# Performance work log

Hardware: AMD Instinct MI355X
Metric: run time of the kernel (lower is better)

Reference implementation:

```python
import jax, jax.numpy as jnp
import numpy as np

L, D, DH, NH, P = 12, 768, 64, 12, 16
B, H_IMG, W_IMG = 16, 384, 384
MAX_GRID = 64


def setup_inputs() -> dict:
    key = jax.random.key(0)
    ks = jax.random.split(key, 10)
    r = lambda k, shp: (0.02 * jax.random.normal(k, shp, dtype=jnp.float32))
    return {
        "x": jax.random.normal(ks[0], (B, 3, H_IMG, W_IMG), dtype=jnp.float32),
        "conv_w": r(ks[1], (D, 3, P, P)),
        "conv_b": jnp.zeros((D,), jnp.float32),
        "ln_w": jnp.ones((D,), jnp.float32),
        "ln_b": jnp.zeros((D,), jnp.float32),
        "pos_y_emb": r(ks[2], (MAX_GRID, D)),
        "pos_x_emb": r(ks[3], (MAX_GRID, D)),
        "mha_ln_w": jnp.ones((L, D), jnp.float32),
        "mha_ln_b": jnp.zeros((L, D), jnp.float32),
        "qw": r(ks[4], (L, D, D)),
        "kw": r(ks[5], (L, D, D)),
        "vw": r(ks[6], (L, D, D)),
        "ffn_ln_w": jnp.ones((L, D), jnp.float32),
        "ffn_ln_b": jnp.zeros((L, D), jnp.float32),
        "w1": r(ks[7], (L, D, 4 * D)),
        "b1": jnp.zeros((L, 4 * D), jnp.float32),
        "w2": r(ks[8], (L, 4 * D, D)),
        "b2": jnp.zeros((L, D), jnp.float32),
        "x_shift": 0,
        "y_shift": 0,
    }


def _ln(x, w, b):
    m = jnp.mean(x, axis=-1, keepdims=True)
    v = jnp.var(x, axis=-1, keepdims=True)
    return (x - m) * jax.lax.rsqrt(v + 1e-5) * w + b


def reference(x, conv_w, conv_b, ln_w, ln_b, pos_y_emb, pos_x_emb,
              mha_ln_w, mha_ln_b, qw, kw, vw,
              ffn_ln_w, ffn_ln_b, w1, b1, w2, b2, x_shift, y_shift):
    # patch embed: conv + relu, to NHWC, layernorm
    h = jax.lax.conv_general_dilated(x, conv_w, (P, P), 'VALID',
                                     dimension_numbers=('NCHW', 'OIHW', 'NCHW'))
    h = jax.nn.relu(h + conv_b[None, :, None, None])
    h = jnp.transpose(h, (0, 2, 3, 1))  # [B, GH, GW, D]
    h = _ln(h, ln_w, ln_b)
    b, gh, gw, d = h.shape
    n = gh * gw
    # 2D factorized positional embedding, shared layernorm
    pos = (pos_y_emb[jnp.arange(gh) + y_shift][:, None, :]
           + pos_x_emb[jnp.arange(gw) + x_shift][None, :, :])  # [GH, GW, D]
    pos = _ln(pos, ln_w, ln_b).reshape(1, n, d)
    pos_emb = jnp.broadcast_to(pos, (b, n, d))
    t = h.reshape(b, n, d) + pos_emb
    scale = 1.0 / jnp.sqrt(jnp.float32(DH))
    for i in range(L):
        # pre-LN MHA (no output projection, mask=None / pretrain=False)
        tl = _ln(t, mha_ln_w[i], mha_ln_b[i])
        q = (tl @ qw[i]).reshape(b, n, NH, DH).transpose(0, 2, 1, 3)
        k = (tl @ kw[i]).reshape(b, n, NH, DH).transpose(0, 2, 1, 3)
        v = (tl @ vw[i]).reshape(b, n, NH, DH).transpose(0, 2, 1, 3)
        attn = jax.nn.softmax(jnp.einsum('bhqd,bhkd->bhqk', q, k) * scale, axis=-1)
        o = jnp.einsum('bhqk,bhkd->bhqd', attn, v).transpose(0, 2, 1, 3).reshape(b, n, d)
        t = t + o
        fl = _ln(t, ffn_ln_w[i], ffn_ln_b[i])
        t = t + (jax.nn.relu(fl @ w1[i] + b1[i]) @ w2[i] + b2[i])
    return t, pos_emb
```

## Files before the change

kernel.cpp:

```cpp
#include <hip/hip_runtime.h>

typedef unsigned short u16;
typedef __attribute__((ext_vector_type(4))) float f32x4;
typedef __attribute__((ext_vector_type(8))) short s16x8;

__device__ __forceinline__ u16 f2bf(float f) {
    union { float f; unsigned u; } v; v.f = f;
    unsigned r = v.u + 0x7FFFu + ((v.u >> 16) & 1u);
    return (u16)(r >> 16);
}

__device__ __forceinline__ void gload_lds16(const u16* g, u16* l) {
    __builtin_amdgcn_global_load_lds(
        (const __attribute__((address_space(1))) unsigned int*)(g),
        (__attribute__((address_space(3))) unsigned int*)(l),
        16, 0, 0);
}

#define NTOK 9216
#define SEQ  576
#define DMODEL 768
#define DFF  3072
#define NHEAD 12
#define HDIM 64

__global__ __launch_bounds__(256) void convert_bf16_kernel(const float* __restrict__ in,
                                                           u16* __restrict__ out, int n) {
    for (int i = blockIdx.x * 256 + threadIdx.x; i < n; i += gridDim.x * 256)
        out[i] = f2bf(in[i]);
}

__global__ __launch_bounds__(256) void copy_f32_kernel(const float* __restrict__ in,
                                                       float* __restrict__ out, int n4) {
    const float4* a = (const float4*)in;
    float4* o = (float4*)out;
    for (int i = blockIdx.x * 256 + threadIdx.x; i < n4; i += gridDim.x * 256)
        o[i] = a[i];
}

__global__ __launch_bounds__(256) void im2col_kernel(const float* __restrict__ x,
                                                     u16* __restrict__ out) {
    int tok = blockIdx.x;
    int b = tok / SEQ, n = tok % SEQ;
    int gy = n / 24, gx = n % 24;
    int tid = threadIdx.x;
#pragma unroll
    for (int j = 0; j < 3; ++j) {
        int col = tid + j * 256;
        int c = col >> 8, py = (col >> 4) & 15, px = col & 15;
        float v = x[(size_t)((b * 3 + c) * 384 + gy * 16 + py) * 384 + gx * 16 + px];
        out[(size_t)tok * DMODEL + col] = f2bf(v);
    }
}

__global__ __launch_bounds__(256) void transpose_layer_kernel(
        const float* __restrict__ qw, const float* __restrict__ kw, const float* __restrict__ vw,
        const float* __restrict__ w1, const float* __restrict__ w2,
        u16* __restrict__ wTq, u16* __restrict__ wTk, u16* __restrict__ wTv,
        u16* __restrict__ w1T, u16* __restrict__ w2T) {
    int bid = blockIdx.x;
    const float* src; u16* dst; int Kd, Nd, tile;
    if (bid < 1728)      { int m = bid / 576; src = m == 0 ? qw : (m == 1 ? kw : vw);
                           dst = m == 0 ? wTq : (m == 1 ? wTk : wTv); Kd = 768; Nd = 768; tile = bid % 576; }
    else if (bid < 4032) { src = w1; dst = w1T; Kd = 768; Nd = 3072; tile = bid - 1728; }
    else                 { src = w2; dst = w2T; Kd = 3072; Nd = 768; tile = bid - 4032; }
    int ntx = Nd / 32;
    int tk = (tile / ntx) * 32, tn = (tile % ntx) * 32;
    __shared__ float ts[32][33];
    int tx = threadIdx.x & 31, ty = threadIdx.x >> 5;
#pragma unroll
    for (int j = 0; j < 32; j += 8)
        ts[ty + j][tx] = src[(size_t)(tk + ty + j) * Nd + tn + tx];
    __syncthreads();
#pragma unroll
    for (int j = 0; j < 32; j += 8)
        dst[(size_t)(tn + ty + j) * Kd + tk + tx] = f2bf(ts[tx][ty + j]);
}

__global__ __launch_bounds__(256) void ln_bf16_kernel(const float* __restrict__ X,
                                                      const float* __restrict__ w,
                                                      const float* __restrict__ b,
                                                      u16* __restrict__ Y) {
    int row = blockIdx.x, tid = threadIdx.x;
    const float* x = X + (size_t)row * DMODEL;
    float v0 = x[tid], v1 = x[tid + 256], v2 = x[tid + 512];
    float s = v0 + v1 + v2, sq = v0 * v0 + v1 * v1 + v2 * v2;
#pragma unroll
    for (int off = 32; off >= 1; off >>= 1) { s += __shfl_down(s, off); sq += __shfl_down(sq, off); }
    __shared__ float red[8];
    if ((tid & 63) == 0) { red[tid >> 6] = s; red[4 + (tid >> 6)] = sq; }
    __syncthreads();
    float S = red[0] + red[1] + red[2] + red[3];
    float Q = red[4] + red[5] + red[6] + red[7];
    float mean = S * (1.f / DMODEL);
    float var = Q * (1.f / DMODEL) - mean * mean;
    float inv = rsqrtf(var + 1e-5f);
    u16* y = Y + (size_t)row * DMODEL;
    y[tid]       = f2bf((v0 - mean) * inv * w[tid]       + b[tid]);
    y[tid + 256] = f2bf((v1 - mean) * inv * w[tid + 256] + b[tid + 256]);
    y[tid + 512] = f2bf((v2 - mean) * inv * w[tid + 512] + b[tid + 512]);
}

__global__ __launch_bounds__(256) void ln_add_pos_kernel(float* __restrict__ T,
                                                         const float* __restrict__ w,
                                                         const float* __restrict__ b,
                                                         const float* __restrict__ posln) {
    int row = blockIdx.x, tid = threadIdx.x;
    float* x = T + (size_t)row * DMODEL;
    const float* p = posln + (size_t)(row % SEQ) * DMODEL;
    float v0 = x[tid], v1 = x[tid + 256], v2 = x[tid + 512];
    float s = v0 + v1 + v2, sq = v0 * v0 + v1 * v1 + v2 * v2;
#pragma unroll
    for (int off = 32; off >= 1; off >>= 1) { s += __shfl_down(s, off); sq += __shfl_down(sq, off); }
    __shared__ float red[8];
    if ((tid & 63) == 0) { red[tid >> 6] = s; red[4 + (tid >> 6)] = sq; }
    __syncthreads();
    float S = red[0] + red[1] + red[2] + red[3];
    float Q = red[4] + red[5] + red[6] + red[7];
    float mean = S * (1.f / DMODEL);
    float var = Q * (1.f / DMODEL) - mean * mean;
    float inv = rsqrtf(var + 1e-5f);
    x[tid]       = (v0 - mean) * inv * w[tid]       + b[tid]       + p[tid];
    x[tid + 256] = (v1 - mean) * inv * w[tid + 256] + b[tid + 256] + p[tid + 256];
    x[tid + 512] = (v2 - mean) * inv * w[tid + 512] + b[tid + 512] + p[tid + 512];
}

__global__ __launch_bounds__(256) void pos_ln_kernel(const float* __restrict__ py,
                                                     const float* __restrict__ px,
                                                     const float* __restrict__ w,
                                                     const float* __restrict__ b,
                                                     const int* __restrict__ xs_p,
                                                     const int* __restrict__ ys_p,
                                                     float* __restrict__ posln,
                                                     float* __restrict__ out2) {
    int row = blockIdx.x;
    int gy = row / 24, gx = row % 24;
    int ys = ys_p[0], xs = xs_p[0];
    int tid = threadIdx.x;
    float v[3]; float s = 0.f, sq = 0.f;
#pragma unroll
    for (int j = 0; j < 3; ++j) {
        int c = tid + j * 256;
        v[j] = py[(size_t)(gy + ys) * DMODEL + c] + px[(size_t)(gx + xs) * DMODEL + c];
        s += v[j]; sq += v[j] * v[j];
    }
#pragma unroll
    for (int off = 32; off >= 1; off >>= 1) { s += __shfl_down(s, off); sq += __shfl_down(sq, off); }
    __shared__ float red[8];
    if ((tid & 63) == 0) { red[tid >> 6] = s; red[4 + (tid >> 6)] = sq; }
    __syncthreads();
    float S = red[0] + red[1] + red[2] + red[3];
    float Q = red[4] + red[5] + red[6] + red[7];
    float mean = S * (1.f / DMODEL);
    float var = Q * (1.f / DMODEL) - mean * mean;
    float inv = rsqrtf(var + 1e-5f);
#pragma unroll
    for (int j = 0; j < 3; ++j) {
        int c = tid + j * 256;
        float y = (v[j] - mean) * inv * w[c] + b[c];
        posln[(size_t)row * DMODEL + c] = y;
        for (int bb = 0; bb < 16; ++bb)
            out2[((size_t)bb * SEQ + row) * DMODEL + c] = y;
    }
}

#define EPI_CONV 0
#define EPI_BF16 1
#define EPI_VT   2
#define EPI_FFN1 3
#define EPI_FFN2 4

template <int EPI>
__global__ __launch_bounds__(256) void gemm_bt(const u16* __restrict__ A,
                                               const u16* __restrict__ Bt,
                                               float* __restrict__ outF,
                                               u16* __restrict__ outB,
                                               const float* __restrict__ bias,
                                               int M, int N, int K) {
    __shared__ __align__(16) u16 As[128 * 32];
    __shared__ __align__(16) u16 Bs[128 * 32];
    const int tid = threadIdx.x;
    const int wave = tid >> 6, lane = tid & 63;
    const int c_lo = lane & 15, c_hi = lane >> 4;
    const int m0 = blockIdx.x * 128, n0 = blockIdx.y * 128;
    const int wr = (wave >> 1) * 64, wc = (wave & 1) * 64;
    f32x4 acc[4][4] = {};
    for (int k0 = 0; k0 < K; k0 += 32) {
        __syncthreads();
#pragma unroll
        for (int i = 0; i < 2; ++i) {
            int c = i * 256 + tid;
            int row = c >> 2, slot = (c & 3) * 8;
            u16* lbase_a = (u16*)((char*)As + (i * 4 + wave) * 1024);
            u16* lbase_b = (u16*)((char*)Bs + (i * 4 + wave) * 1024);
            gload_lds16(A + (size_t)(m0 + row) * K + k0 + slot, lbase_a);
            gload_lds16(Bt + (size_t)(n0 + row) * K + k0 + slot, lbase_b);
        }
        __syncthreads();
        s16x8 af[4], bf[4];
#pragma unroll
        for (int m = 0; m < 4; ++m)
            af[m] = *(const s16x8*)&As[(wr + m * 16 + c_lo) * 32 + c_hi * 8];
#pragma unroll
        for (int n = 0; n < 4; ++n)
            bf[n] = *(const s16x8*)&Bs[(wc + n * 16 + c_lo) * 32 + c_hi * 8];
#pragma unroll
        for (int m = 0; m < 4; ++m)
#pragma unroll
            for (int n = 0; n < 4; ++n)
                acc[m][n] = __builtin_amdgcn_mfma_f32_16x16x32_bf16(af[m], bf[n], acc[m][n], 0, 0, 0);
    }
#pragma unroll
    for (int m = 0; m < 4; ++m)
#pragma unroll
        for (int n = 0; n < 4; ++n)
#pragma unroll
            for (int r = 0; r < 4; ++r) {
                int grow = m0 + wr + m * 16 + c_hi * 4 + r;
                int gcol = n0 + wc + n * 16 + c_lo;
                float v = acc[m][n][r];
                if (EPI == EPI_CONV) {
                    v += bias[gcol]; v = fmaxf(v, 0.f);
                    outF[(size_t)grow * N + gcol] = v;
                } else if (EPI == EPI_BF16) {
                    outB[(size_t)grow * N + gcol] = f2bf(v);
                } else if (EPI == EPI_VT) {
                    int b = grow / SEQ, nt = grow % SEQ;
                    int h = gcol >> 6, dh = gcol & 63;
                    outB[(size_t)(((b * NHEAD + h) << 6) + dh) * SEQ + nt] = f2bf(v);
                } else if (EPI == EPI_FFN1) {
                    v += bias[gcol]; v = fmaxf(v, 0.f);
                    outB[(size_t)grow * N + gcol] = f2bf(v);
                } else if (EPI == EPI_FFN2) {
                    outF[(size_t)grow * DMODEL + gcol] += v + bias[gcol];
                }
            }
}

__global__ __launch_bounds__(256) void attn_kernel(const u16* __restrict__ Qb,
                                                   const u16* __restrict__ Kb,
                                                   const u16* __restrict__ Vt,
                                                   float* __restrict__ T) {
    int bid = blockIdx.x;
    int qt = bid % 9, h = (bid / 9) % NHEAD, b = bid / (9 * NHEAD);
    int q0 = qt * 64;
    const int tid = threadIdx.x, wave = tid >> 6, lane = tid & 63;
    const int c_lo = lane & 15, c_hi = lane >> 4;
    __shared__ __align__(16) u16 Qs[64][72];
    __shared__ __align__(16) u16 Ks[64][72];
    __shared__ __align__(16) u16 Vs[64][72];
    __shared__ __align__(16) u16 Ps[4][16][72];
#pragma unroll
    for (int i = 0; i < 2; ++i) {
        int c = i * 256 + tid, row = c >> 3, slot = (c & 7) * 8;
        *(s16x8*)&Qs[row][slot] =
            *(const s16x8*)(Qb + ((size_t)(b * SEQ + q0 + row) * DMODEL + h * HDIM + slot));
    }
    f32x4 o[4] = {};
    float mrun[4], lrun[4];
#pragma unroll
    for (int r = 0; r < 4; ++r) { mrun[r] = -1e30f; lrun[r] = 0.f; }
    for (int t2 = 0; t2 < 9; ++t2) {
        int kv0 = t2 * 64;
        __syncthreads();
#pragma unroll
        for (int i = 0; i < 2; ++i) {
            int c = i * 256 + tid, row = c >> 3, slot = (c & 7) * 8;
            *(s16x8*)&Ks[row][slot] =
                *(const s16x8*)(Kb + ((size_t)(b * SEQ + kv0 + row) * DMODEL + h * HDIM + slot));
            *(s16x8*)&Vs[row][slot] =
                *(const s16x8*)(Vt + ((size_t)((b * NHEAD + h) * HDIM + row) * SEQ + kv0 + slot));
        }
        __syncthreads();
        f32x4 s[4] = {};
        s16x8 aq[2];
#pragma unroll
        for (int ks = 0; ks < 2; ++ks)
            aq[ks] = *(const s16x8*)&Qs[wave * 16 + c_lo][ks * 32 + c_hi * 8];
#pragma unroll
        for (int nf = 0; nf < 4; ++nf)
#pragma unroll
            for (int ks = 0; ks < 2; ++ks) {
                s16x8 bk = *(const s16x8*)&Ks[nf * 16 + c_lo][ks * 32 + c_hi * 8];
                s[nf] = __builtin_amdgcn_mfma_f32_16x16x32_bf16(aq[ks], bk, s[nf], 0, 0, 0);
            }
#pragma unroll
        for (int nf = 0; nf < 4; ++nf)
#pragma unroll
            for (int r = 0; r < 4; ++r) s[nf][r] *= 0.125f;
        float mx[4];
#pragma unroll
        for (int r = 0; r < 4; ++r)
            mx[r] = fmaxf(fmaxf(s[0][r], s[1][r]), fmaxf(s[2][r], s[3][r]));
#pragma unroll
        for (int off = 1; off < 16; off <<= 1)
#pragma unroll
            for (int r = 0; r < 4; ++r) mx[r] = fmaxf(mx[r], __shfl_xor(mx[r], off));
        float alpha[4];
#pragma unroll
        for (int r = 0; r < 4; ++r) {
            float mn = fmaxf(mrun[r], mx[r]);
            alpha[r] = __expf(mrun[r] - mn);
            mrun[r] = mn;
            lrun[r] *= alpha[r];
        }
        float ls[4] = {0.f, 0.f, 0.f, 0.f};
        u16 pb[4][4];
#pragma unroll
        for (int nf = 0; nf < 4; ++nf)
#pragma unroll
            for (int r = 0; r < 4; ++r) {
                float p = __expf(s[nf][r] - mrun[r]);
                ls[r] += p;
                pb[nf][r] = f2bf(p);
            }
#pragma unroll
        for (int off = 1; off < 16; off <<= 1)
#pragma unroll
            for (int r = 0; r < 4; ++r) ls[r] += __shfl_xor(ls[r], off);
#pragma unroll
        for (int r = 0; r < 4; ++r) lrun[r] += ls[r];
#pragma unroll
        for (int df = 0; df < 4; ++df)
#pragma unroll
            for (int r = 0; r < 4; ++r) o[df][r] *= alpha[r];
#pragma unroll
        for (int nf = 0; nf < 4; ++nf)
#pragma unroll
            for (int r = 0; r < 4; ++r)
                Ps[wave][c_hi * 4 + r][c_lo + nf * 16] = pb[nf][r];
        asm volatile("s_waitcnt lgkmcnt(0)" ::: "memory");
        s16x8 pa[2];
#pragma unroll
        for (int ks = 0; ks < 2; ++ks)
            pa[ks] = *(const s16x8*)&Ps[wave][c_lo][ks * 32 + c_hi * 8];
#pragma unroll
        for (int df = 0; df < 4; ++df)
#pragma unroll
            for (int ks = 0; ks < 2; ++ks) {
                s16x8 bv = *(const s16x8*)&Vs[df * 16 + c_lo][ks * 32 + c_hi * 8];
                o[df] = __builtin_amdgcn_mfma_f32_16x16x32_bf16(pa[ks], bv, o[df], 0, 0, 0);
            }
    }
#pragma unroll
    for (int df = 0; df < 4; ++df)
#pragma unroll
        for (int r = 0; r < 4; ++r) {
            int grow = b * SEQ + q0 + wave * 16 + c_hi * 4 + r;
            int gcol = h * HDIM + df * 16 + c_lo;
            T[(size_t)grow * DMODEL + gcol] += o[df][r] / lrun[r];
        }
}

extern "C" void kernel_launch(void* const* d_in, const int* in_sizes, int n_in,
                              void* d_out, int out_size, void* d_ws, size_t ws_size,
                              hipStream_t stream) {
    (void)in_sizes; (void)n_in; (void)out_size; (void)ws_size;
    const float* x        = (const float*)d_in[0];
    const float* conv_w   = (const float*)d_in[1];
    const float* conv_b   = (const float*)d_in[2];
    const float* ln_w     = (const float*)d_in[3];
    const float* ln_b     = (const float*)d_in[4];
    const float* pos_y    = (const float*)d_in[5];
    const float* pos_x    = (const float*)d_in[6];
    const float* mha_ln_w = (const float*)d_in[7];
    const float* mha_ln_b = (const float*)d_in[8];
    const float* qw       = (const float*)d_in[9];
    const float* kw       = (const float*)d_in[10];
    const float* vw       = (const float*)d_in[11];
    const float* ffn_ln_w = (const float*)d_in[12];
    const float* ffn_ln_b = (const float*)d_in[13];
    const float* w1       = (const float*)d_in[14];
    const float* b1       = (const float*)d_in[15];
    const float* w2       = (const float*)d_in[16];
    const float* b2       = (const float*)d_in[17];
    const int*   xs       = (const int*)d_in[18];
    const int*   ys       = (const int*)d_in[19];
    float* out1 = (float*)d_out;
    float* out2 = out1 + (size_t)NTOK * DMODEL;

    size_t off = 0;
    char* ws = (char*)d_ws;
    auto carve = [&](size_t bytes) { char* p = ws + off; off += (bytes + 255) & ~(size_t)255; return p; };
    u16* wTq = (u16*)carve((size_t)768 * 768 * 2);
    u16* wTk = (u16*)carve((size_t)768 * 768 * 2);
    u16* wTv = (u16*)carve((size_t)768 * 768 * 2);
    u16* w1T = (u16*)carve((size_t)DFF * DMODEL * 2);
    u16* w2T = (u16*)carve((size_t)DMODEL * DFF * 2);
    float* t  = (float*)carve((size_t)NTOK * DMODEL * 4);
    u16* tl   = (u16*)carve((size_t)NTOK * DMODEL * 2);
    u16* qb   = (u16*)carve((size_t)NTOK * DMODEL * 2);
    u16* kb   = (u16*)carve((size_t)NTOK * DMODEL * 2);
    u16* vT   = (u16*)carve((size_t)NTOK * DMODEL * 2);
    u16* hb   = (u16*)carve((size_t)NTOK * DFF * 2);
    float* posln = (float*)carve((size_t)SEQ * DMODEL * 4);
    u16* cw   = wTq;
    u16* im2c = hb;

    convert_bf16_kernel<<<1152, 256, 0, stream>>>(conv_w, cw, 768 * 768);
    im2col_kernel<<<NTOK, 256, 0, stream>>>(x, im2c);
    gemm_bt<EPI_CONV><<<dim3(72, 6), 256, 0, stream>>>(im2c, cw, t, nullptr, conv_b, NTOK, DMODEL, DMODEL);
    pos_ln_kernel<<<SEQ, 256, 0, stream>>>(pos_y, pos_x, ln_w, ln_b, xs, ys, posln, out2);
    ln_add_pos_kernel<<<NTOK, 256, 0, stream>>>(t, ln_w, ln_b, posln);

    for (int i = 0; i < 12; ++i) {
        transpose_layer_kernel<<<6336, 256, 0, stream>>>(
            qw + (size_t)i * 768 * 768, kw + (size_t)i * 768 * 768, vw + (size_t)i * 768 * 768,
            w1 + (size_t)i * 768 * DFF, w2 + (size_t)i * DFF * 768,
            wTq, wTk, wTv, w1T, w2T);
        ln_bf16_kernel<<<NTOK, 256, 0, stream>>>(t, mha_ln_w + i * DMODEL, mha_ln_b + i * DMODEL, tl);
        gemm_bt<EPI_BF16><<<dim3(72, 6), 256, 0, stream>>>(tl, wTq, nullptr, qb, nullptr, NTOK, DMODEL, DMODEL);
        gemm_bt<EPI_BF16><<<dim3(72, 6), 256, 0, stream>>>(tl, wTk, nullptr, kb, nullptr, NTOK, DMODEL, DMODEL);
        gemm_bt<EPI_VT>  <<<dim3(72, 6), 256, 0, stream>>>(tl, wTv, nullptr, vT, nullptr, NTOK, DMODEL, DMODEL);
        attn_kernel<<<16 * NHEAD * 9, 256, 0, stream>>>(qb, kb, vT, t);
        ln_bf16_kernel<<<NTOK, 256, 0, stream>>>(t, ffn_ln_w + i * DMODEL, ffn_ln_b + i * DMODEL, tl);
        gemm_bt<EPI_FFN1><<<dim3(72, 24), 256, 0, stream>>>(tl, w1T, nullptr, hb, b1 + i * DFF, NTOK, DFF, DMODEL);
        gemm_bt<EPI_FFN2><<<dim3(72, 6), 256, 0, stream>>>(hb, w2T, t, nullptr, b2 + i * DMODEL, NTOK, DMODEL, DFF);
    }
    copy_f32_kernel<<<2048, 256, 0, stream>>>(t, out1, (NTOK * DMODEL) / 4);
}
```

Measured before the change: 3.816 ms.

## Rewrite GEMM with triple-buffered async LDS pipeline, swizzle, and fused QKV

Replaces the single-stage 128x128 GEMM with a 512-thread 128x256 tile kernel. It uses a triple-buffered global-to-LDS pipeline with explicit vmcnt waits, an XOR-swizzled LDS layout to avoid bank conflicts, and K-steps of 64. The Q, K and V projections are merged into one launch over a concatenated weight buffer, with a per-block epilogue that routes output to the right tensor. The aim is to hide memory latency behind MFMA work and cut per-step barrier overhead and launch count, at the cost of higher LDS use (144KB per block) and lower occupancy.

```diff
diff --git a/kernel.cpp b/kernel.cpp
--- a/kernel.cpp
+++ b/kernel.cpp
@@ -165,69 +165,119 @@
 }
 
 #define EPI_CONV 0
-#define EPI_BF16 1
-#define EPI_VT   2
+#define EPI_QKV  1
 #define EPI_FFN1 3
 #define EPI_FFN2 4
 
 template <int EPI>
-__global__ __launch_bounds__(256) void gemm_bt(const u16* __restrict__ A,
-                                               const u16* __restrict__ Bt,
-                                               float* __restrict__ outF,
-                                               u16* __restrict__ outB,
-                                               const float* __restrict__ bias,
-                                               int M, int N, int K) {
-    __shared__ __align__(16) u16 As[128 * 32];
-    __shared__ __align__(16) u16 Bs[128 * 32];
+__global__ __launch_bounds__(512, 2) void gemm3(const u16* __restrict__ A,
+                                                const u16* __restrict__ Bt,
+                                                float* __restrict__ outF,
+                                                u16* __restrict__ outB,
+                                                u16* __restrict__ outB2,
+                                                u16* __restrict__ outB3,
+                                                const float* __restrict__ bias,
+                                                int M, int N, int K) {
+    __shared__ __align__(16) u16 lds[3 * 24576];
     const int tid = threadIdx.x;
     const int wave = tid >> 6, lane = tid & 63;
     const int c_lo = lane & 15, c_hi = lane >> 4;
-    const int m0 = blockIdx.x * 128, n0 = blockIdx.y * 128;
-    const int wr = (wave >> 1) * 64, wc = (wave & 1) * 64;
+    const int wm = wave >> 2, wn = wave & 3;
+    const int m0 = blockIdx.x * 128, n0 = blockIdx.y * 256;
+
+    int rowA[2], kkA[2], rowB[4], kkB[4];
+#pragma unroll
+    for (int r = 0; r < 2; ++r) {
+        int L = r * 8192 + tid * 16;
+        int P = L ^ ((L >> 3) & 0x70);
+        rowA[r] = P >> 7; kkA[r] = (P & 127) >> 1;
+    }
+#pragma unroll
+    for (int r = 0; r < 4; ++r) {
+        int L = r * 8192 + tid * 16;
+        int P = L ^ ((L >> 3) & 0x70);
+        rowB[r] = P >> 7; kkB[r] = (P & 127) >> 1;
+    }
+    const int NT = K >> 6;
     f32x4 acc[4][4] = {};
-    for (int k0 = 0; k0 < K; k0 += 32) {
-        __syncthreads();
-#pragma unroll
-        for (int i = 0; i < 2; ++i) {
-            int c = i * 256 + tid;
-            int row = c >> 2, slot = (c & 3) * 8;
-            u16* lbase_a = (u16*)((char*)As + (i * 4 + wave) * 1024);
-            u16* lbase_b = (u16*)((char*)Bs + (i * 4 + wave) * 1024);
-            gload_lds16(A + (size_t)(m0 + row) * K + k0 + slot, lbase_a);
-            gload_lds16(Bt + (size_t)(n0 + row) * K + k0 + slot, lbase_b);
-        }
-        __syncthreads();
-        s16x8 af[4], bf[4];
-#pragma unroll
-        for (int m = 0; m < 4; ++m)
-            af[m] = *(const s16x8*)&As[(wr + m * 16 + c_lo) * 32 + c_hi * 8];
-#pragma unroll
-        for (int n = 0; n < 4; ++n)
-            bf[n] = *(const s16x8*)&Bs[(wc + n * 16 + c_lo) * 32 + c_hi * 8];
-#pragma unroll
-        for (int m = 0; m < 4; ++m)
-#pragma unroll
-            for (int n = 0; n < 4; ++n)
-                acc[m][n] = __builtin_amdgcn_mfma_f32_16x16x32_bf16(af[m], bf[n], acc[m][n], 0, 0, 0);
-    }
-#pragma unroll
-    for (int m = 0; m < 4; ++m)
-#pragma unroll
-        for (int n = 0; n < 4; ++n)
+
+    auto stage = [&](int t) {
+        u16* buf = lds + (t % 3) * 24576;
+        int k0 = t << 6;
+#pragma unroll
+        for (int r = 0; r < 2; ++r)
+            gload_lds16(A + (size_t)(m0 + rowA[r]) * K + k0 + kkA[r],
+                        buf + r * 4096 + wave * 512);
+#pragma unroll
+        for (int r = 0; r < 4; ++r)
+            gload_lds16(Bt + (size_t)(n0 + rowB[r]) * K + k0 + kkB[r],
+                        buf + 8192 + r * 4096 + wave * 512);
+    };
+
+    stage(0); stage(1);
+    asm volatile("s_waitcnt vmcnt(6)" ::: "memory");
+    __builtin_amdgcn_s_barrier();
+    __builtin_amdgcn_sched_barrier(0);
+
+    for (int t = 0; t < NT; ++t) {
+        if (t + 2 < NT) stage(t + 2);
+        const u16* Ab = lds + (t % 3) * 24576;
+        const u16* Bb = Ab + 8192;
+        s16x8 af[4][2], bf[4][2];
+#pragma unroll
+        for (int mf = 0; mf < 4; ++mf)
+#pragma unroll
+            for (int ks = 0; ks < 2; ++ks) {
+                int by = (wm * 64 + mf * 16 + c_lo) * 128 + (ks * 32 + c_hi * 8) * 2;
+                by ^= (by >> 3) & 0x70;
+                af[mf][ks] = *(const s16x8*)((const char*)Ab + by);
+            }
+#pragma unroll
+        for (int nf = 0; nf < 4; ++nf)
+#pragma unroll
+            for (int ks = 0; ks < 2; ++ks) {
+                int by = (wn * 64 + nf * 16 + c_lo) * 128 + (ks * 32 + c_hi * 8) * 2;
+                by ^= (by >> 3) & 0x70;
+                bf[nf][ks] = *(const s16x8*)((const char*)Bb + by);
+            }
+        __builtin_amdgcn_s_setprio(1);
+#pragma unroll
+        for (int mf = 0; mf < 4; ++mf)
+#pragma unroll
+            for (int nf = 0; nf < 4; ++nf)
+#pragma unroll
+                for (int ks = 0; ks < 2; ++ks)
+                    acc[mf][nf] = __builtin_amdgcn_mfma_f32_16x16x32_bf16(
+                        af[mf][ks], bf[nf][ks], acc[mf][nf], 0, 0, 0);
+        __builtin_amdgcn_s_setprio(0);
+        if (t + 2 < NT) { asm volatile("s_waitcnt vmcnt(6)" ::: "memory"); }
+        else            { asm volatile("s_waitcnt vmcnt(0)" ::: "memory"); }
+        __builtin_amdgcn_s_barrier();
+        __builtin_amdgcn_sched_barrier(0);
+    }
+
+#pragma unroll
+    for (int mf = 0; mf < 4; ++mf)
+#pragma unroll
+        for (int nf = 0; nf < 4; ++nf)
 #pragma unroll
             for (int r = 0; r < 4; ++r) {
-                int grow = m0 + wr + m * 16 + c_hi * 4 + r;
-                int gcol = n0 + wc + n * 16 + c_lo;
-                float v = acc[m][n][r];
+                int grow = m0 + wm * 64 + mf * 16 + c_hi * 4 + r;
+                int gcol = n0 + wn * 64 + nf * 16 + c_lo;
+                float v = acc[mf][nf][r];
                 if (EPI == EPI_CONV) {
                     v += bias[gcol]; v = fmaxf(v, 0.f);
                     outF[(size_t)grow * N + gcol] = v;
-                } else if (EPI == EPI_BF16) {
-                    outB[(size_t)grow * N + gcol] = f2bf(v);
-                } else if (EPI == EPI_VT) {
-                    int b = grow / SEQ, nt = grow % SEQ;
-                    int h = gcol >> 6, dh = gcol & 63;
-                    outB[(size_t)(((b * NHEAD + h) << 6) + dh) * SEQ + nt] = f2bf(v);
+                } else if (EPI == EPI_QKV) {
+                    int sel = n0 / 768;
+                    int lcol = gcol - sel * 768;
+                    if (sel == 0)      outB [(size_t)grow * 768 + lcol] = f2bf(v);
+                    else if (sel == 1) outB2[(size_t)grow * 768 + lcol] = f2bf(v);
+                    else {
+                        int b = grow / SEQ, nt = grow % SEQ;
+                        int h = lcol >> 6, dh = lcol & 63;
+                        outB3[(size_t)(((b * NHEAD + h) << 6) + dh) * SEQ + nt] = f2bf(v);
+                    }
                 } else if (EPI == EPI_FFN1) {
                     v += bias[gcol]; v = fmaxf(v, 0.f);
                     outB[(size_t)grow * N + gcol] = f2bf(v);
@@ -382,9 +432,7 @@
     size_t off = 0;
     char* ws = (char*)d_ws;
     auto carve = [&](size_t bytes) { char* p = ws + off; off += (bytes + 255) & ~(size_t)255; return p; };
-    u16* wTq = (u16*)carve((size_t)768 * 768 * 2);
-    u16* wTk = (u16*)carve((size_t)768 * 768 * 2);
-    u16* wTv = (u16*)carve((size_t)768 * 768 * 2);
+    u16* wTqkv = (u16*)carve((size_t)3 * 768 * 768 * 2);
     u16* w1T = (u16*)carve((size_t)DFF * DMODEL * 2);
     u16* w2T = (u16*)carve((size_t)DMODEL * DFF * 2);
     float* t  = (float*)carve((size_t)NTOK * DMODEL * 4);
@@ -394,12 +442,16 @@
     u16* vT   = (u16*)carve((size_t)NTOK * DMODEL * 2);
     u16* hb   = (u16*)carve((size_t)NTOK * DFF * 2);
     float* posln = (float*)carve((size_t)SEQ * DMODEL * 4);
-    u16* cw   = wTq;
+    u16* wTq = wTqkv;
+    u16* wTk = wTqkv + (size_t)768 * 768;
+    u16* wTv = wTqkv + (size_t)2 * 768 * 768;
+    u16* cw   = wTqkv;
     u16* im2c = hb;
 
     convert_bf16_kernel<<<1152, 256, 0, stream>>>(conv_w, cw, 768 * 768);
     im2col_kernel<<<NTOK, 256, 0, stream>>>(x, im2c);
-    gemm_bt<EPI_CONV><<<dim3(72, 6), 256, 0, stream>>>(im2c, cw, t, nullptr, conv_b, NTOK, DMODEL, DMODEL);
+    gemm3<EPI_CONV><<<dim3(72, 3), 512, 0, stream>>>(im2c, cw, t, nullptr, nullptr, nullptr,
+                                                     conv_b, NTOK, DMODEL, DMODEL);
     pos_ln_kernel<<<SEQ, 256, 0, stream>>>(pos_y, pos_x, ln_w, ln_b, xs, ys, posln, out2);
     ln_add_pos_kernel<<<NTOK, 256, 0, stream>>>(t, ln_w, ln_b, posln);
 
@@ -409,13 +461,14 @@
             w1 + (size_t)i * 768 * DFF, w2 + (size_t)i * DFF * 768,
             wTq, wTk, wTv, w1T, w2T);
         ln_bf16_kernel<<<NTOK, 256, 0, stream>>>(t, mha_ln_w + i * DMODEL, mha_ln_b + i * DMODEL, tl);
-        gemm_bt<EPI_BF16><<<dim3(72, 6), 256, 0, stream>>>(tl, wTq, nullptr, qb, nullptr, NTOK, DMODEL, DMODEL);
-        gemm_bt<EPI_BF16><<<dim3(72, 6), 256, 0, stream>>>(tl, wTk, nullptr, kb, nullptr, NTOK, DMODEL, DMODEL);
-        gemm_bt<EPI_VT>  <<<dim3(72, 6), 256, 0, stream>>>(tl, wTv, nullptr, vT, nullptr, NTOK, DMODEL, DMODEL);
+        gemm3<EPI_QKV><<<dim3(72, 9), 512, 0, stream>>>(tl, wTqkv, nullptr, qb, kb, vT,
+                                                        nullptr, NTOK, 3 * DMODEL, DMODEL);
         attn_kernel<<<16 * NHEAD * 9, 256, 0, stream>>>(qb, kb, vT, t);
         ln_bf16_kernel<<<NTOK, 256, 0, stream>>>(t, ffn_ln_w + i * DMODEL, ffn_ln_b + i * DMODEL, tl);
-        gemm_bt<EPI_FFN1><<<dim3(72, 24), 256, 0, stream>>>(tl, w1T, nullptr, hb, b1 + i * DFF, NTOK, DFF, DMODEL);
-        gemm_bt<EPI_FFN2><<<dim3(72, 6), 256, 0, stream>>>(hb, w2T, t, nullptr, b2 + i * DMODEL, NTOK, DMODEL, DFF);
+        gemm3<EPI_FFN1><<<dim3(72, 12), 512, 0, stream>>>(tl, w1T, nullptr, hb, nullptr, nullptr,
+                                                          b1 + (size_t)i * DFF, NTOK, DFF, DMODEL);
+        gemm3<EPI_FFN2><<<dim3(72, 3), 512, 0, stream>>>(hb, w2T, t, nullptr, nullptr, nullptr,
+                                                         b2 + (size_t)i * DMODEL, NTOK, DMODEL, DFF);
     }
     copy_f32_kernel<<<2048, 256, 0, stream>>>(t, out1, (NTOK * DMODEL) / 4);
 }
```

Measured after the change: 3.256 ms. 1.17x faster.
